# Optimization experiments

Measured on AMD Instinct MI355X. Metric: run time of the kernel, lower is better.

The kernel has to match this reference:

```python
import jax, jax.numpy as jnp
import numpy as np


def setup_inputs() -> dict:
    key = jax.random.key(0)
    k1, k2 = jax.random.split(key)
    codes = jax.random.normal(k1, (32, 512, 64, 64), dtype=jnp.float32)
    # semantic map: integer {0,1} per segment channel at input resolution
    sem = jax.random.randint(k2, (32, 8, 256, 256), 0, 2, dtype=jnp.int32)
    # zero out the last segment channel so the empty-mask fallback branch is exercised
    sem = sem.at[:, -1].set(0)
    return {"codes": codes, "sem": sem}


def _nearest_downsample(sem, hs, ws):
    # matches F.interpolate(mode='nearest'): out[i] = in[floor(i * H_in / H_out)]
    H, W = sem.shape[2], sem.shape[3]
    ih = (jnp.arange(hs) * H) // hs
    iw = (jnp.arange(ws) * W) // ws
    return sem[:, :, ih[:, None], iw[None, :]]  # [bs, s, hs, ws]


def reference(codes, sem):
    bs, cs, hs, ws = codes.shape
    s_size = sem.shape[1]
    segmap = _nearest_downsample(sem, hs, ws)          # [bs, s, hs, ws] int
    mask = (segmap != 0).astype(codes.dtype)           # bool-as-float mask
    area = mask.sum(axis=(-2, -1))                     # [bs, s]
    # masked per-channel sums over spatial dims (fused segment reduce)
    sums = jnp.einsum('bchw,bshw->bsc', codes, mask)   # [bs, s, c]
    seg_mean = sums / jnp.maximum(area, 1.0)[..., None]
    # fallback for empty masks: global per-channel spatial mean (calc_mean_std mean)
    glob_mean = codes.mean(axis=(2, 3))                # [bs, c]
    codes_vector = jnp.where(area[..., None] > 0, seg_mean, glob_mean[:, None, :])
    return codes_vector.reshape(bs, -1)[:, :, None, None]  # [bs, s*c, 1, 1]
```

## Files before the change

### kernel.cpp

```cpp
#include <hip/hip_runtime.h>
#include <hip/hip_bf16.h>


#define BS    32
#define CS    512
#define SEG   8
#define HS    64
#define WS    64
#define HW    (HS*WS)
#define SEMH  256
#define SEMW  256
#define NCHUNK 16
#define CPB   2

__global__ __launch_bounds__(256) void mask_area_kernel(
    const int* __restrict__ sem,
    unsigned char* __restrict__ mask8,
    int* __restrict__ partial)
{
    const int blk   = blockIdx.x;
    const int b     = blk >> 4;
    const int chunk = blk & (NCHUNK - 1);
    const int t     = threadIdx.x;

    const int hw = chunk * 256 + t;
    const int h  = hw >> 6;
    const int w  = hw & 63;
    const int* p = sem + (size_t)b * SEG * SEMH * SEMW + (h * 4) * SEMW + (w * 4);

    unsigned int m = 0;
#pragma unroll
    for (int s = 0; s < SEG; ++s)
        if (p[s * (SEMH * SEMW)] != 0) m |= (1u << s);
    mask8[b * HW + hw] = (unsigned char)m;

    __shared__ int redc[4][SEG];
    const int lane = t & 63, wv = t >> 6;
#pragma unroll
    for (int s = 0; s < SEG; ++s) {
        unsigned long long bal = __ballot((m >> s) & 1u);
        if (lane == 0) redc[wv][s] = __popcll(bal);
    }
    __syncthreads();
    if (t < SEG)
        partial[(b * NCHUNK + chunk) * SEG + t] =
            redc[0][t] + redc[1][t] + redc[2][t] + redc[3][t];
}

__global__ __launch_bounds__(64) void seg_mean_kernel(
    const float* __restrict__ codes,
    const unsigned char* __restrict__ mask8,
    const int* __restrict__ partial,
    float* __restrict__ out)
{
    const int blk = blockIdx.x;
    const int b   = blk >> 8;
    const int c0  = (blk & 255) * CPB;
    const int l   = threadIdx.x;

    const float* src = codes + ((size_t)b * CS + c0) * HW;
    const unsigned char* mb = mask8 + b * HW;

    float acc[CPB][SEG];
    float gl[CPB];
#pragma unroll
    for (int cc = 0; cc < CPB; ++cc) {
        gl[cc] = 0.0f;
#pragma unroll
        for (int s = 0; s < SEG; ++s) acc[cc][s] = 0.0f;
    }

#pragma unroll
    for (int i = 0; i < 16; ++i) {
        const int hw = i * 256 + l * 4;
        const unsigned int m4 = *reinterpret_cast<const unsigned int*>(mb + hw);
        const float4 v0 = *reinterpret_cast<const float4*>(src + hw);
        const float4 v1 = *reinterpret_cast<const float4*>(src + HW + hw);
        const float va[CPB][4] = { { v0.x, v0.y, v0.z, v0.w },
                                   { v1.x, v1.y, v1.z, v1.w } };
#pragma unroll
        for (int p = 0; p < 4; ++p) {
            const unsigned int lo = (m4 >> (8 * p)) & 0xFu;
            const unsigned int hi = (m4 >> (8 * p + 4)) & 0xFu;
            const unsigned int slo = ((unsigned int)__mul24((int)lo, 0x00204081)) & 0x01010101u;
            const unsigned int shi = ((unsigned int)__mul24((int)hi, 0x00204081)) & 0x01010101u;
            float w[SEG];
            w[0] = (float)( slo        & 0xffu);
            w[1] = (float)((slo >> 8)  & 0xffu);
            w[2] = (float)((slo >> 16) & 0xffu);
            w[3] = (float)( slo >> 24        );
            w[4] = (float)( shi        & 0xffu);
            w[5] = (float)((shi >> 8)  & 0xffu);
            w[6] = (float)((shi >> 16) & 0xffu);
            w[7] = (float)( shi >> 24        );
#pragma unroll
            for (int cc = 0; cc < CPB; ++cc) {
                const float val = va[cc][p];
                gl[cc] += val;
#pragma unroll
                for (int s = 0; s < SEG; ++s)
                    acc[cc][s] = fmaf(val, w[s], acc[cc][s]);
            }
        }
    }

#pragma unroll
    for (int off = 32; off; off >>= 1) {
#pragma unroll
        for (int cc = 0; cc < CPB; ++cc) {
            gl[cc] += __shfl_xor(gl[cc], off);
#pragma unroll
            for (int s = 0; s < SEG; ++s)
                acc[cc][s] += __shfl_xor(acc[cc][s], off);
        }
    }

    if (l < SEG) {
        int ai = 0;
#pragma unroll
        for (int k = 0; k < NCHUNK; ++k)
            ai += partial[(b * NCHUNK + k) * SEG + l];
        const float a = (float)ai;
#pragma unroll
        for (int cc = 0; cc < CPB; ++cc) {
            float seg = 0.0f;
#pragma unroll
            for (int s = 0; s < SEG; ++s)
                seg = (l == s) ? acc[cc][s] : seg;
            out[b * (SEG * CS) + l * CS + (c0 + cc)] =
                (a > 0.0f) ? (seg / a) : (gl[cc] * (1.0f / (float)HW));
        }
    }
}

extern "C" void kernel_launch(void* const* d_in, const int* in_sizes, int n_in,
                              void* d_out, int out_size, void* d_ws, size_t ws_size,
                              hipStream_t stream) {
    const float* codes = (const float*)d_in[0];
    const int*   sem   = (const int*)d_in[1];
    float*       out   = (float*)d_out;

    unsigned char* mask8   = (unsigned char*)d_ws;
    int*           partial = (int*)((char*)d_ws + BS * HW);

    mask_area_kernel<<<BS * NCHUNK, 256, 0, stream>>>(sem, mask8, partial);
    seg_mean_kernel<<<BS * CS / CPB, 64, 0, stream>>>(codes, mask8, partial, out);
}
```

Before: 57.39 us.

## Rework mask kernel to one wave per row and widen channels per block

```diff
diff --git a/kernel.cpp b/kernel.cpp
--- a/kernel.cpp
+++ b/kernel.cpp
@@ -2,49 +2,48 @@
 #include <hip/hip_bf16.h>
 
 
-#define BS    32
-#define CS    512
-#define SEG   8
-#define HS    64
-#define WS    64
-#define HW    (HS*WS)
-#define SEMH  256
-#define SEMW  256
-#define NCHUNK 16
-#define CPB   2
+#define BS     32
+#define CS     512
+#define SEG    8
+#define HS     64
+#define WS     64
+#define HW     (HS*WS)
+#define SEMH   256
+#define SEMW   256
+#define NCHUNK 64
+#define CPB    4
 
-__global__ __launch_bounds__(256) void mask_area_kernel(
+typedef float f32x4 __attribute__((ext_vector_type(4)));
+
+__global__ __launch_bounds__(64) void mask_area_kernel(
     const int* __restrict__ sem,
     unsigned char* __restrict__ mask8,
     int* __restrict__ partial)
 {
     const int blk   = blockIdx.x;
-    const int b     = blk >> 4;
+    const int b     = blk >> 6;
     const int chunk = blk & (NCHUNK - 1);
-    const int t     = threadIdx.x;
+    const int l     = threadIdx.x;
 
-    const int hw = chunk * 256 + t;
-    const int h  = hw >> 6;
-    const int w  = hw & 63;
-    const int* p = sem + (size_t)b * SEG * SEMH * SEMW + (h * 4) * SEMW + (w * 4);
+    const int hw = chunk * 64 + l;
+    const int* p = sem + (size_t)b * SEG * SEMH * SEMW + (chunk * 4) * SEMW + l * 4;
 
     unsigned int m = 0;
 #pragma unroll
     for (int s = 0; s < SEG; ++s)
-        if (p[s * (SEMH * SEMW)] != 0) m |= (1u << s);
+        if (__builtin_nontemporal_load(p + s * (SEMH * SEMW)) != 0) m |= (1u << s);
     mask8[b * HW + hw] = (unsigned char)m;
 
-    __shared__ int redc[4][SEG];
-    const int lane = t & 63, wv = t >> 6;
+    unsigned long long bal[SEG];
 #pragma unroll
-    for (int s = 0; s < SEG; ++s) {
-        unsigned long long bal = __ballot((m >> s) & 1u);
-        if (lane == 0) redc[wv][s] = __popcll(bal);
+    for (int s = 0; s < SEG; ++s) bal[s] = __ballot((m >> s) & 1u);
+
+    if (l < SEG) {
+        unsigned long long mine = 0;
+#pragma unroll
+        for (int s = 0; s < SEG; ++s) mine = (l == s) ? bal[s] : mine;
+        partial[(b * NCHUNK + chunk) * SEG + l] = __popcll(mine);
     }
-    __syncthreads();
-    if (t < SEG)
-        partial[(b * NCHUNK + chunk) * SEG + t] =
-            redc[0][t] + redc[1][t] + redc[2][t] + redc[3][t];
 }
 
 __global__ __launch_bounds__(64) void seg_mean_kernel(
@@ -54,8 +53,8 @@
     float* __restrict__ out)
 {
     const int blk = blockIdx.x;
-    const int b   = blk >> 8;
-    const int c0  = (blk & 255) * CPB;
+    const int b   = blk >> 7;
+    const int c0  = (blk & 127) * CPB;
     const int l   = threadIdx.x;
 
     const float* src = codes + ((size_t)b * CS + c0) * HW;
@@ -74,34 +73,32 @@
     for (int i = 0; i < 16; ++i) {
         const int hw = i * 256 + l * 4;
         const unsigned int m4 = *reinterpret_cast<const unsigned int*>(mb + hw);
-        const float4 v0 = *reinterpret_cast<const float4*>(src + hw);
-        const float4 v1 = *reinterpret_cast<const float4*>(src + HW + hw);
-        const float va[CPB][4] = { { v0.x, v0.y, v0.z, v0.w },
-                                   { v1.x, v1.y, v1.z, v1.w } };
+        f32x4 v[CPB];
 #pragma unroll
-        for (int p = 0; p < 4; ++p) {
-            const unsigned int lo = (m4 >> (8 * p)) & 0xFu;
-            const unsigned int hi = (m4 >> (8 * p + 4)) & 0xFu;
-            const unsigned int slo = ((unsigned int)__mul24((int)lo, 0x00204081)) & 0x01010101u;
-            const unsigned int shi = ((unsigned int)__mul24((int)hi, 0x00204081)) & 0x01010101u;
-            float w[SEG];
-            w[0] = (float)( slo        & 0xffu);
-            w[1] = (float)((slo >> 8)  & 0xffu);
-            w[2] = (float)((slo >> 16) & 0xffu);
-            w[3] = (float)( slo >> 24        );
-            w[4] = (float)( shi        & 0xffu);
-            w[5] = (float)((shi >> 8)  & 0xffu);
-            w[6] = (float)((shi >> 16) & 0xffu);
-            w[7] = (float)( shi >> 24        );
+        for (int cc = 0; cc < CPB; ++cc)
+            v[cc] = __builtin_nontemporal_load(
+                reinterpret_cast<const f32x4*>(src + cc * HW + hw));
+
+#pragma unroll
+        for (int s = 0; s < SEG; ++s) {
+            const unsigned int w4 = (m4 >> s) & 0x01010101u;
+            const float w0 = (float)( w4        & 0xffu);
+            const float w1 = (float)((w4 >> 8)  & 0xffu);
+            const float w2 = (float)((w4 >> 16) & 0xffu);
+            const float w3 = (float)( w4 >> 24        );
 #pragma unroll
             for (int cc = 0; cc < CPB; ++cc) {
-                const float val = va[cc][p];
-                gl[cc] += val;
-#pragma unroll
-                for (int s = 0; s < SEG; ++s)
-                    acc[cc][s] = fmaf(val, w[s], acc[cc][s]);
+                float a0 = acc[cc][s];
+                a0 = fmaf(v[cc].x, w0, a0);
+                a0 = fmaf(v[cc].y, w1, a0);
+                a0 = fmaf(v[cc].z, w2, a0);
+                a0 = fmaf(v[cc].w, w3, a0);
+                acc[cc][s] = a0;
             }
         }
+#pragma unroll
+        for (int cc = 0; cc < CPB; ++cc)
+            gl[cc] += (v[cc].x + v[cc].y) + (v[cc].z + v[cc].w);
     }
 
 #pragma unroll
@@ -115,20 +112,26 @@
         }
     }
 
+    const int seg = l & 7;
+    const int cg  = l >> 3;
+    int ai = 0;
+#pragma unroll
+    for (int k = 0; k < 8; ++k)
+        ai += partial[(b * NCHUNK + cg * 8 + k) * SEG + seg];
+    ai += __shfl_xor(ai, 8);
+    ai += __shfl_xor(ai, 16);
+    ai += __shfl_xor(ai, 32);
+    const float a = (float)ai;
+
     if (l < SEG) {
-        int ai = 0;
-#pragma unroll
-        for (int k = 0; k < NCHUNK; ++k)
-            ai += partial[(b * NCHUNK + k) * SEG + l];
-        const float a = (float)ai;
 #pragma unroll
         for (int cc = 0; cc < CPB; ++cc) {
-            float seg = 0.0f;
+            float segsum = 0.0f;
 #pragma unroll
             for (int s = 0; s < SEG; ++s)
-                seg = (l == s) ? acc[cc][s] : seg;
+                segsum = (l == s) ? acc[cc][s] : segsum;
             out[b * (SEG * CS) + l * CS + (c0 + cc)] =
-                (a > 0.0f) ? (seg / a) : (gl[cc] * (1.0f / (float)HW));
+                (a > 0.0f) ? (segsum / a) : (gl[cc] * (1.0f / (float)HW));
         }
     }
 }
@@ -143,6 +146,6 @@
     unsigned char* mask8   = (unsigned char*)d_ws;
     int*           partial = (int*)((char*)d_ws + BS * HW);
 
-    mask_area_kernel<<<BS * NCHUNK, 256, 0, stream>>>(sem, mask8, partial);
+    mask_area_kernel<<<BS * NCHUNK, 64, 0, stream>>>(sem, mask8, partial);
     seg_mean_kernel<<<BS * CS / CPB, 64, 0, stream>>>(codes, mask8, partial, out);
 }
```

Result: slower. 59.58 us (+3.8%).
